# Performance work log

Measured on AMD Instinct MI355X. Metric: run time of the kernel, lower is better.

The kernel has to match this reference:

```python
import jax, jax.numpy as jnp
import numpy as np

B, T, EMB, H = 8, 1024, 128, 8


def setup_inputs() -> dict:
    key = jax.random.key(0)
    ks = jax.random.split(key, 7)
    s = 0.02
    return {
        "x": jax.random.normal(ks[0], (B, T, EMB), dtype=jnp.float32),
        "mask": jax.random.randint(ks[1], (1, T, T), 0, 2, dtype=jnp.int32),
        "Wk": (jax.random.normal(ks[2], (EMB * H, EMB), dtype=jnp.float32) * s),
        "Wq": (jax.random.normal(ks[3], (EMB * H, EMB), dtype=jnp.float32) * s),
        "Wv": (jax.random.normal(ks[4], (EMB * H, EMB), dtype=jnp.float32) * s),
        "Wu": (jax.random.normal(ks[5], (EMB, EMB * H), dtype=jnp.float32) * s),
        "bu": (jax.random.normal(ks[6], (EMB,), dtype=jnp.float32) * s),
    }


def reference(x, mask, Wk, Wq, Wv, Wu, bu):
    b, t, e = x.shape  # e == emb; per-head dim also == emb in this module
    h = Wk.shape[0] // e
    # projections: (b,t,e) @ (e, h*e) -> (b,t,h,e) -> (b,h,t,e)
    q = (x @ Wq.T).reshape(b, t, h, e).transpose(0, 2, 1, 3)
    k = (x @ Wk.T).reshape(b, t, h, e).transpose(0, 2, 1, 3)
    v = (x @ Wv.T).reshape(b, t, h, e).transpose(0, 2, 1, 3)
    scale = e ** 0.25  # torch scales q and k each by e**(1/4)
    dot = jnp.einsum('bhqe,bhke->bhqk', q / scale, k / scale)
    # causal mask: strictly-upper triangle (offset=1) set to -inf FIRST
    causal = jnp.triu(jnp.ones((t, t), dtype=bool), k=1)
    dot = jnp.where(causal, -jnp.inf, dot)
    # padding mask: where mask==0 set to -1e9 (overwrites -inf where overlapping)
    dot = jnp.where(mask[:, None] == 0, jnp.float32(-1e9), dot)
    attn = jax.nn.softmax(dot, axis=-1)
    out = jnp.einsum('bhqk,bhke->bhqe', attn, v)
    out = out.transpose(0, 2, 1, 3).reshape(b, t, h * e)
    return out @ Wu.T + bu
```

## Files before the change

### kernel.cpp

```cpp
#include <hip/hip_runtime.h>

#define Bn 8
#define Hn 8
#define Tn 1024
#define Dn 128

typedef __attribute__((ext_vector_type(8))) short bf16x8;
typedef __attribute__((ext_vector_type(4))) float f32x4;

typedef __attribute__((address_space(3))) unsigned int lds_as_t;
typedef __attribute__((address_space(1))) const unsigned int glb_as_t;

static __device__ __forceinline__ void gload_lds16(const unsigned short* g, unsigned short* l) {
    __builtin_amdgcn_global_load_lds((glb_as_t*)g, (lds_as_t*)l, 16, 0, 0);
}
static __device__ __forceinline__ void gload_lds16b(const char* g, char* l) {
    __builtin_amdgcn_global_load_lds((glb_as_t*)g, (lds_as_t*)l, 16, 0, 0);
}

static __device__ __forceinline__ unsigned short f2bf(float f) {
    union { float f; unsigned int u; } v; v.f = f;
    unsigned int u = v.u;
    return (unsigned short)((u + 0x7FFFu + ((u >> 16) & 1u)) >> 16);
}
static __device__ __forceinline__ int pack_bf16_trunc(float lo, float hi) {
    union { float f; unsigned int u; } a, b;
    a.f = lo; b.f = hi;
    return (int)__builtin_amdgcn_perm(b.u, a.u, 0x07060302u);
}

__global__ __launch_bounds__(256) void prep_kernel(
    const float* __restrict__ x,  const float* __restrict__ Wq,
    const float* __restrict__ Wk, const float* __restrict__ Wv,
    const float* __restrict__ Wu, const int* __restrict__ mask,
    const float* __restrict__ bu, float* __restrict__ outp,
    unsigned short* __restrict__ xb,  unsigned short* __restrict__ wqB,
    unsigned short* __restrict__ wkB, unsigned short* __restrict__ wvB,
    unsigned short* __restrict__ wuF, unsigned long long* __restrict__ bits)
{
    const int blk = blockIdx.x;
    const int tid = threadIdx.x;

    if (blk < 1408) {
        const float* in; unsigned short* out; int i4;
        if (blk < 1024)      { in = x;  out = xb;  i4 = blk * 256 + tid; }
        else if (blk < 1152) { in = Wq; out = wqB; i4 = (blk - 1024) * 256 + tid; }
        else if (blk < 1280) { in = Wk; out = wkB; i4 = (blk - 1152) * 256 + tid; }
        else                 { in = Wv; out = wvB; i4 = (blk - 1280) * 256 + tid; }
        float4 f = ((const float4*)in)[i4];
        ushort4 o;
        o.x = f2bf(f.x); o.y = f2bf(f.y); o.z = f2bf(f.z); o.w = f2bf(f.w);
        int base = i4 * 4;
        int row = base >> 7, col = base & 127;
        int scol = (((col >> 3) ^ (row & 15)) << 3) | (col & 7);
        *(ushort4*)(out + row * 128 + scol) = o;
    } else if (blk < 1536) {
        if (tid < 128) {
            int id = (blk - 1408) * 128 + tid;
            int lane_ = id & 63;
            int fid = id >> 6;
            int nt = fid & 7, ks = (fid >> 3) & 3, h = fid >> 5;
            int row = nt * 16 + (lane_ & 15);
            int col = h * 128 + ks * 32 + (lane_ >> 4) * 8;
            const float* src = Wu + (size_t)row * 1024 + col;
            float4 f0 = *(const float4*)(src);
            float4 f1 = *(const float4*)(src + 4);
            unsigned short o[8];
            o[0] = f2bf(f0.x); o[1] = f2bf(f0.y); o[2] = f2bf(f0.z); o[3] = f2bf(f0.w);
            o[4] = f2bf(f1.x); o[5] = f2bf(f1.y); o[6] = f2bf(f1.z); o[7] = f2bf(f1.w);
            *(ushort4*)(wuF + (size_t)id * 8)     = *(ushort4*)&o[0];
            *(ushort4*)(wuF + (size_t)id * 8 + 4) = *(ushort4*)&o[4];
        }
    } else if (blk < 2560) {
        int wid  = (blk - 1536) * 4 + (tid >> 6);
        int lane = tid & 63;
#pragma unroll
        for (int i = 0; i < 4; i++) {
            int widx = wid * 4 + i;
            int row = widx >> 4, kt = widx & 15;
            int v = mask[row * Tn + kt * 64 + lane];
            unsigned long long b = __ballot(v != 0);
            if (lane == 0) bits[kt * Tn + row] = b;
        }
    } else {
        int f4 = (blk - 2560) * 1024 + tid * 4;
#pragma unroll
        for (int i = 0; i < 4; i++)
            ((float4*)outp)[f4 + i] = ((const float4*)bu)[(f4 + i) & 31];
    }
}

__global__ __launch_bounds__(256, 1) void qkv_kernel(
    const unsigned short* __restrict__ xb,
    const unsigned short* __restrict__ wqB,
    const unsigned short* __restrict__ wkB,
    const unsigned short* __restrict__ wvB,
    char* __restrict__ Q,
    char* __restrict__ K,
    unsigned short* __restrict__ Vt)
{
    const int bx = blockIdx.x, by = blockIdx.y;
    const int wave = threadIdx.x >> 6;
    const int lane = threadIdx.x & 63;
    const int l16  = lane & 15;
    const int quad = lane >> 4;
    const int wm = wave & 1, wn = wave >> 1;

    __shared__ __align__(16) unsigned short As[128 * 128];
    __shared__ __align__(16) unsigned short Bs[3][128 * 128];
    __shared__ __align__(16) char escr[128 * 144];

    const unsigned short* Ag = xb + (size_t)bx * 128 * 128;
    const unsigned short* Bg0 = wqB + (size_t)by * 128 * 128;
    const unsigned short* Bg1 = wkB + (size_t)by * 128 * 128;
    const unsigned short* Bg2 = wvB + (size_t)by * 128 * 128;

#pragma unroll
    for (int i = 0; i < 8; i++) {
        int base = (wave * 8 + i) * 512;
        gload_lds16(Ag  + base + lane * 8, &As[base]);
        gload_lds16(Bg0 + base + lane * 8, &Bs[0][base]);
    }
    __syncthreads();

    bf16x8 a[4][4];
#pragma unroll
    for (int mt = 0; mt < 4; mt++) {
        int row = wm * 64 + mt * 16 + l16;
#pragma unroll
        for (int ks = 0; ks < 4; ks++)
            a[mt][ks] = *(const bf16x8*)(&As[row * 128 + (((ks * 4 + quad) ^ (row & 15)) << 3)]);
    }

    const int h_ = by;
    const int b_ = bx >> 3;
    f32x4 acc[4][4];

    {
#pragma unroll
        for (int i = 0; i < 8; i++) {
            int base = (wave * 8 + i) * 512;
            gload_lds16(Bg1 + base + lane * 8, &Bs[1][base]);
        }
#pragma unroll
        for (int nt = 0; nt < 4; nt++) {
            int row = wn * 64 + nt * 16 + l16;
            bf16x8 b4[4];
#pragma unroll
            for (int ks = 0; ks < 4; ks++)
                b4[ks] = *(const bf16x8*)(&Bs[0][row * 128 + (((ks * 4 + quad) ^ (row & 15)) << 3)]);
#pragma unroll
            for (int mt = 0; mt < 4; mt++) {
                f32x4 c = {0.f, 0.f, 0.f, 0.f};
#pragma unroll
                for (int ks = 0; ks < 4; ks++)
                    c = __builtin_amdgcn_mfma_f32_16x16x32_bf16(a[mt][ks], b4[ks], c, 0, 0, 0);
                acc[mt][nt] = c;
            }
        }
#pragma unroll
        for (int mt = 0; mt < 4; mt++) {
#pragma unroll
            for (int nt = 0; nt < 4; nt++) {
                int w = __builtin_amdgcn_cvt_pk_fp8_f32(acc[mt][nt][0], acc[mt][nt][1], 0, false);
                w = __builtin_amdgcn_cvt_pk_fp8_f32(acc[mt][nt][2], acc[mt][nt][3], w, true);
                int col = wn * 64 + nt * 16 + l16;
#pragma unroll
                for (int r = 0; r < 4; r++)
                    escr[(wm * 64 + mt * 16 + quad * 4 + r) * 144 + col] = (char)(w >> (8 * r));
            }
        }
        __syncthreads();
        const int f = threadIdx.x;
        int row = f >> 1;
        int t_in = (bx & 7) * 128 + row;
        size_t rowbase = ((size_t)((b_ * Hn + h_) * Tn + t_in)) * 128;
#pragma unroll
        for (int i = 0; i < 4; i++) {
            int c = (f & 1) * 4 + i;
            int4 v = *(const int4*)(escr + row * 144 + c * 16);
            *(int4*)(Q + rowbase + c * 16) = v;
        }
    }

    {
#pragma unroll
        for (int i = 0; i < 8; i++) {
            int base = (wave * 8 + i) * 512;
            gload_lds16(Bg2 + base + lane * 8, &Bs[2][base]);
        }
#pragma unroll
        for (int nt = 0; nt < 4; nt++) {
            int row = wn * 64 + nt * 16 + l16;
            bf16x8 b4[4];
#pragma unroll
            for (int ks = 0; ks < 4; ks++)
                b4[ks] = *(const bf16x8*)(&Bs[1][row * 128 + (((ks * 4 + quad) ^ (row & 15)) << 3)]);
#pragma unroll
            for (int mt = 0; mt < 4; mt++) {
                f32x4 c = {0.f, 0.f, 0.f, 0.f};
#pragma unroll
                for (int ks = 0; ks < 4; ks++)
                    c = __builtin_amdgcn_mfma_f32_16x16x32_bf16(a[mt][ks], b4[ks], c, 0, 0, 0);
                acc[mt][nt] = c;
            }
        }
        __syncthreads();
#pragma unroll
        for (int mt = 0; mt < 4; mt++) {
#pragma unroll
            for (int nt = 0; nt < 4; nt++) {
                int w = __builtin_amdgcn_cvt_pk_fp8_f32(acc[mt][nt][0], acc[mt][nt][1], 0, false);
                w = __builtin_amdgcn_cvt_pk_fp8_f32(acc[mt][nt][2], acc[mt][nt][3], w, true);
                int col = wn * 64 + nt * 16 + l16;
#pragma unroll
                for (int r = 0; r < 4; r++)
                    escr[(wm * 64 + mt * 16 + quad * 4 + r) * 144 + col] = (char)(w >> (8 * r));
            }
        }
        __syncthreads();
        const int f = threadIdx.x;
        int row = f >> 1;
        int t_in = (bx & 7) * 128 + row;
        size_t rowbase = ((size_t)((b_ * Hn + h_) * Tn + t_in)) * 128;
#pragma unroll
        for (int i = 0; i < 4; i++) {
            int c = (f & 1) * 4 + i;
            int4 v = *(const int4*)(escr + row * 144 + c * 16);
            int cc = c ^ (row & 7);
            *(int4*)(K + rowbase + cc * 16) = v;
        }
    }

    {
#pragma unroll
        for (int nt = 0; nt < 4; nt++) {
            int row = wn * 64 + nt * 16 + l16;
            bf16x8 b4[4];
#pragma unroll
            for (int ks = 0; ks < 4; ks++)
                b4[ks] = *(const bf16x8*)(&Bs[2][row * 128 + (((ks * 4 + quad) ^ (row & 15)) << 3)]);
#pragma unroll
            for (int mt = 0; mt < 4; mt++) {
                f32x4 c = {0.f, 0.f, 0.f, 0.f};
#pragma unroll
                for (int ks = 0; ks < 4; ks++)
                    c = __builtin_amdgcn_mfma_f32_16x16x32_bf16(a[mt][ks], b4[ks], c, 0, 0, 0);
                acc[mt][nt] = c;
            }
        }
#pragma unroll
        for (int mt = 0; mt < 4; mt++) {
            int m_base = bx * 128 + wm * 64 + mt * 16 + quad * 4;
            int t0 = m_base & 1023;
#pragma unroll
            for (int nt = 0; nt < 4; nt++) {
                int e_ = wn * 64 + nt * 16 + l16;
                int kt_ = t0 >> 6, tc0 = t0 & 63;
                size_t off = ((((size_t)(b_ * Hn + h_) * 16 + kt_) * 128 + e_) << 6)
                           + ((((tc0 >> 3) ^ (e_ & 7)) << 3) | (tc0 & 7));
                ushort4 v4;
                v4.x = f2bf(acc[mt][nt][0]); v4.y = f2bf(acc[mt][nt][1]);
                v4.z = f2bf(acc[mt][nt][2]); v4.w = f2bf(acc[mt][nt][3]);
                *(ushort4*)(Vt + off) = v4;
            }
        }
    }
}

__global__ __launch_bounds__(256, 2) void attn_kernel(
    const char* __restrict__ Q,
    const char* __restrict__ K,
    const unsigned short* __restrict__ Vt,
    const unsigned long long* __restrict__ mbits,
    const unsigned short* __restrict__ wuF,
    float* __restrict__ out)
{
    const int id   = blockIdx.x;
    const int qb   = (id & 7) ^ (7 * ((id >> 8) & 1));
    const int bh   = (id >> 3) & 63;
    const int wave = threadIdx.x >> 6;
    const int lane = threadIdx.x & 63;
    const int l16  = lane & 15;
    const int quad = lane >> 4;

    __shared__ __align__(16) char kbuf[2][64 * 128];
    __shared__ __align__(16) unsigned short vbuf[2][128 * 64];

    const char* Qb = Q  + (size_t)bh * Tn * Dn;
    const char* Kb = K  + (size_t)bh * Tn * Dn;
    const unsigned short* Vb = Vt + (size_t)bh * (16 * 128 * 64);

    const int blkkt = 2 * qb + 1;
    const int q0w   = qb * 128 + wave * 32;
    const int q0s[2] = { q0w, q0w + 16 };
    const int wkmax = (q0w + 31) >> 6;

    long qf[2][4];
#pragma unroll
    for (int st = 0; st < 2; st++)
#pragma unroll
        for (int ks = 0; ks < 4; ks++)
            qf[st][ks] = *(const long*)(Qb + (size_t)(q0s[st] + l16) * 128 + ks * 32 + quad * 8);

    bf16x8 ones;
#pragma unroll
    for (int j = 0; j < 8; j++) ones[j] = (short)0x3F80;

    f32x4 o[2][8];
#pragma unroll
    for (int st = 0; st < 2; st++)
#pragma unroll
        for (int et = 0; et < 8; et++) o[st][et] = (f32x4){0.f, 0.f, 0.f, 0.f};
    f32x4 lacc[2];
    lacc[0] = (f32x4){0.f, 0.f, 0.f, 0.f};
    lacc[1] = (f32x4){0.f, 0.f, 0.f, 0.f};

    const float SL = 0.12752041570284543f;

    const int idx0 = (l16 << 2) + ((quad & 1) << 7);
    const int idx1 = idx0 + 64;
    const bool hiQ = (quad >> 1) != 0;

#pragma unroll
    for (int i = 0; i < 2; i++) {
        int base = (wave * 2 + i) * 1024;
        gload_lds16b(Kb + base + lane * 16, &kbuf[0][base]);
    }
#pragma unroll
    for (int i = 0; i < 4; i++) {
        int base = (wave * 4 + i) * 512;
        gload_lds16(Vb + base + lane * 8, &vbuf[0][base]);
    }

    for (int kt = 0; kt <= blkkt; kt++) {
        const int cur = kt & 1;
        __syncthreads();

        if (kt < blkkt) {
            const char* Kg = Kb + (kt + 1) * (64 * 128);
            const unsigned short* Vg = Vb + (kt + 1) * (128 * 64);
#pragma unroll
            for (int i = 0; i < 2; i++) {
                int base = (wave * 2 + i) * 1024;
                gload_lds16b(Kg + base + lane * 16, &kbuf[cur ^ 1][base]);
            }
#pragma unroll
            for (int i = 0; i < 4; i++) {
                int base = (wave * 4 + i) * 512;
                gload_lds16(Vg + base + lane * 8, &vbuf[cur ^ 1][base]);
            }
        }

        if (kt <= wkmax) {
            unsigned long long mw[2];
            mw[0] = mbits[kt * Tn + q0s[0] + l16];
            mw[1] = mbits[kt * Tn + q0s[1] + l16];

            f32x4 s[2][4];
#pragma unroll
            for (int nt = 0; nt < 4; nt++) {
                int row = nt * 16 + l16;
                long a4[4];
#pragma unroll
                for (int ks = 0; ks < 4; ks++) {
                    int c = ks * 2 + (quad >> 1);
                    a4[ks] = *(const long*)(&kbuf[cur][row * 128 + (((c ^ (row & 7)) << 4) | ((quad & 1) << 3))]);
                }
#pragma unroll
                for (int st = 0; st < 2; st++) {
                    f32x4 c = {0.f, 0.f, 0.f, 0.f};
#pragma unroll
                    for (int ks = 0; ks < 4; ks++)
                        c = __builtin_amdgcn_mfma_f32_16x16x32_fp8_fp8(a4[ks], qf[st][ks], c, 0, 0, 0);
                    s[st][nt] = c;
                }
            }

            const int kc0 = kt * 64;
            bf16x8 pf[2][2];
#pragma unroll
            for (int st = 0; st < 2; st++) {
                const int qglob = q0s[st] + l16;
                int w[4][2];
#pragma unroll
                for (int nt = 0; nt < 4; nt++) {
                    float pv[4];
#pragma unroll
                    for (int r = 0; r < 4; r++) {
                        int bit = nt * 16 + quad * 4 + r;
                        bool live = ((mw[st] >> bit) & 1ULL) && (kc0 + bit <= qglob);
                        pv[r] = live ? __builtin_amdgcn_exp2f(s[st][nt][r] * SL) : 0.f;
                    }
                    w[nt][0] = pack_bf16_trunc(pv[0], pv[1]);
                    w[nt][1] = pack_bf16_trunc(pv[2], pv[3]);
                }
#pragma unroll
                for (int k2 = 0; k2 < 2; k2++) {
                    union { int i[4]; bf16x8 v; } u;
#pragma unroll
                    for (int d = 0; d < 4; d++) {
                        int idx = (d < 2) ? idx0 : idx1;
                        int va = __builtin_amdgcn_ds_bpermute(idx, w[2 * k2][d & 1]);
                        int vb = __builtin_amdgcn_ds_bpermute(idx, w[2 * k2 + 1][d & 1]);
                        u.i[d] = hiQ ? vb : va;
                    }
                    pf[st][k2] = u.v;
                }
            }

#pragma unroll
            for (int st = 0; st < 2; st++)
#pragma unroll
                for (int k2 = 0; k2 < 2; k2++)
                    lacc[st] = __builtin_amdgcn_mfma_f32_16x16x32_bf16(pf[st][k2], ones, lacc[st], 0, 0, 0);

#pragma unroll
            for (int et = 0; et < 8; et++) {
                int row = et * 16 + l16;
#pragma unroll
                for (int k2 = 0; k2 < 2; k2++) {
                    bf16x8 b = *(const bf16x8*)(&vbuf[cur][row * 64 + (((k2 * 4 + quad) ^ (l16 & 7)) << 3)]);
                    o[0][et] = __builtin_amdgcn_mfma_f32_16x16x32_bf16(pf[0][k2], b, o[0][et], 0, 0, 0);
                    o[1][et] = __builtin_amdgcn_mfma_f32_16x16x32_bf16(pf[1][k2], b, o[1][et], 0, 0, 0);
                }
            }
        }
    }

    __syncthreads();
    {
        bool deg = false;
#pragma unroll
        for (int st = 0; st < 2; st++)
#pragma unroll
            for (int r = 0; r < 4; r++) deg |= (lacc[st][r] == 0.f);
        if (__ballot(deg) != 0ULL) {
            unsigned short* pb = (unsigned short*)((char*)kbuf + wave * 2304);
            unsigned short dsel[2][4];
#pragma unroll
            for (int st = 0; st < 2; st++)
#pragma unroll
                for (int r = 0; r < 4; r++)
                    dsel[st][r] = (lacc[st][r] == 0.f) ? (unsigned short)0x3F80 : (unsigned short)0;
            for (int kt = 0; kt < 16; kt++) {
#pragma unroll
                for (int st = 0; st < 2; st++) {
                    int qrow = q0s[st] + quad * 4;
                    unsigned long long mw2[4];
#pragma unroll
                    for (int r = 0; r < 4; r++) mw2[r] = mbits[kt * Tn + qrow + r];
#pragma unroll
                    for (int nt = 0; nt < 4; nt++) {
                        int bi = nt * 16 + l16;
#pragma unroll
                        for (int r = 0; r < 4; r++)
                            pb[(quad * 4 + r) * 72 + bi] = ((mw2[r] >> bi) & 1ULL) ? (unsigned short)0 : dsel[st][r];
                    }
                    bf16x8 pf[2];
#pragma unroll
                    for (int k2 = 0; k2 < 2; k2++)
                        pf[k2] = *(const bf16x8*)(&pb[l16 * 72 + k2 * 32 + quad * 8]);
#pragma unroll
                    for (int k2 = 0; k2 < 2; k2++)
                        lacc[st] = __builtin_amdgcn_mfma_f32_16x16x32_bf16(pf[k2], ones, lacc[st], 0, 0, 0);
                    const unsigned short* Vg = Vb + kt * (128 * 64);
#pragma unroll
                    for (int et = 0; et < 8; et++) {
#pragma unroll
                        for (int k2 = 0; k2 < 2; k2++) {
                            bf16x8 b = *(const bf16x8*)(Vg + (et * 16 + l16) * 64 + (((k2 * 4 + quad) ^ (l16 & 7)) << 3));
                            o[st][et] = __builtin_amdgcn_mfma_f32_16x16x32_bf16(pf[k2], b, o[st][et], 0, 0, 0);
                        }
                    }
                }
            }
        }
    }

    const int b_ = bh >> 3, h_ = bh & 7;
    const unsigned short* wf = wuF + (size_t)h_ * (4 * 8 * 64 * 8);
#pragma unroll
    for (int st = 0; st < 2; st++) {
        unsigned short* tile = (unsigned short*)((char*)vbuf + wave * 4608);
#pragma unroll
        for (int r = 0; r < 4; r++) {
            float inv = 1.f / lacc[st][r];
            int row = quad * 4 + r;
#pragma unroll
            for (int et = 0; et < 8; et++)
                tile[row * 144 + et * 16 + l16] = f2bf(o[st][et][r] * inv);
        }

        bf16x8 a4[4];
#pragma unroll
        for (int ks = 0; ks < 4; ks++)
            a4[ks] = *(const bf16x8*)(&tile[l16 * 144 + ks * 32 + quad * 8]);

        f32x4 acc2[8];
#pragma unroll
        for (int nt = 0; nt < 8; nt++) acc2[nt] = (f32x4){0.f, 0.f, 0.f, 0.f};
#pragma unroll
        for (int ks = 0; ks < 4; ks++) {
#pragma unroll
            for (int nt = 0; nt < 8; nt++) {
                bf16x8 b = *(const bf16x8*)(wf + ((size_t)(ks * 8 + nt) * 64 + lane) * 8);
                acc2[nt] = __builtin_amdgcn_mfma_f32_16x16x32_bf16(a4[ks], b, acc2[nt], 0, 0, 0);
            }
        }

#pragma unroll
        for (int nt = 0; nt < 8; nt++) {
            int n = nt * 16 + l16;
#pragma unroll
            for (int r = 0; r < 4; r++) {
                int q = q0s[st] + quad * 4 + r;
                atomicAdd(&out[(size_t)(b_ * Tn + q) * Dn + n], acc2[nt][r]);
            }
        }
    }
}

extern "C" void kernel_launch(void* const* d_in, const int* in_sizes, int n_in,
                              void* d_out, int out_size, void* d_ws, size_t ws_size,
                              hipStream_t stream) {
    const float* x   = (const float*)d_in[0];
    const int* mask  = (const int*)d_in[1];
    const float* Wk  = (const float*)d_in[2];
    const float* Wq  = (const float*)d_in[3];
    const float* Wv  = (const float*)d_in[4];
    const float* Wu  = (const float*)d_in[5];
    const float* bu  = (const float*)d_in[6];
    float* out = (float*)d_out;

    char* ws = (char*)d_ws;
    unsigned short* xb  = (unsigned short*)ws; ws += (size_t)8192 * 128 * 2;
    unsigned short* wqB = (unsigned short*)ws; ws += (size_t)1024 * 128 * 2;
    unsigned short* wkB = (unsigned short*)ws; ws += (size_t)1024 * 128 * 2;
    unsigned short* wvB = (unsigned short*)ws; ws += (size_t)1024 * 128 * 2;
    unsigned short* wuF = (unsigned short*)ws; ws += (size_t)128 * 1024 * 2;
    char* Qf  = ws; ws += (size_t)64 * 1024 * 128;
    char* Kf  = ws; ws += (size_t)64 * 1024 * 128;
    unsigned short* Vtw = (unsigned short*)ws; ws += (size_t)64 * 1024 * 128 * 2;
    unsigned long long* mb = (unsigned long long*)ws; ws += (size_t)1024 * 16 * 8;

    prep_kernel<<<dim3(2816), 256, 0, stream>>>(x, Wq, Wk, Wv, Wu, mask, bu, out,
                                                xb, wqB, wkB, wvB, wuF, mb);
    qkv_kernel<<<dim3(64, 8), 256, 0, stream>>>(xb, wqB, wkB, wvB, Qf, Kf, Vtw);
    attn_kernel<<<dim3(512), 256, 0, stream>>>(Qf, Kf, Vtw, mb, wuF, out);
}
```

Measured before the change: 147.7 us.

## Fuse prep, QKV projection and attention into one persistent kernel with grid barriers

Merges the three launches into a single persistent kernel of 512 blocks that loops over the prep work, then the QKV projection work items, then attention, separated by flag-based grid barriers. The QKV stage is split into 1536 work items (one weight matrix each) instead of 512 items that each computed Q, K and V, which lowers LDS use so two blocks can be resident per CU. The aim is to remove launch gaps and tail effects between kernels. It relies on all 512 blocks being co-resident; the barrier tokens are fixed constants and the flags are never reset, so the barriers can pass immediately on a second call if the workspace keeps the old values. Launch bounds of 2 blocks per CU may also cap registers for the attention stage.

Result: slower. 497.4 us (+236.8%).

```diff
diff --git a/kernel.cpp b/kernel.cpp
--- a/kernel.cpp
+++ b/kernel.cpp
@@ -29,493 +29,431 @@
     return (int)__builtin_amdgcn_perm(b.u, a.u, 0x07060302u);
 }
 
-__global__ __launch_bounds__(256) void prep_kernel(
+static __device__ __forceinline__ void grid_barrier(unsigned* flags, unsigned token) {
+    __syncthreads();
+    __threadfence();
+    if (threadIdx.x == 0)
+        __hip_atomic_store(&flags[blockIdx.x], token, __ATOMIC_RELEASE, __HIP_MEMORY_SCOPE_AGENT);
+    const int i0 = threadIdx.x, i1 = threadIdx.x + 256;
+    while (__hip_atomic_load(&flags[i0], __ATOMIC_ACQUIRE, __HIP_MEMORY_SCOPE_AGENT) != token)
+        __builtin_amdgcn_s_sleep(1);
+    while (__hip_atomic_load(&flags[i1], __ATOMIC_ACQUIRE, __HIP_MEMORY_SCOPE_AGENT) != token)
+        __builtin_amdgcn_s_sleep(1);
+    __syncthreads();
+    __threadfence();
+}
+
+__global__ __launch_bounds__(256, 2) void mega_kernel(
     const float* __restrict__ x,  const float* __restrict__ Wq,
     const float* __restrict__ Wk, const float* __restrict__ Wv,
     const float* __restrict__ Wu, const int* __restrict__ mask,
-    const float* __restrict__ bu, float* __restrict__ outp,
+    const float* __restrict__ bu, float* __restrict__ out,
     unsigned short* __restrict__ xb,  unsigned short* __restrict__ wqB,
     unsigned short* __restrict__ wkB, unsigned short* __restrict__ wvB,
-    unsigned short* __restrict__ wuF, unsigned long long* __restrict__ bits)
+    unsigned short* __restrict__ wuF, char* __restrict__ Qf,
+    char* __restrict__ Kf, unsigned short* __restrict__ Vtw,
+    unsigned long long* __restrict__ mbits, unsigned* __restrict__ flags)
 {
-    const int blk = blockIdx.x;
-    const int tid = threadIdx.x;
-
-    if (blk < 1408) {
-        const float* in; unsigned short* out; int i4;
-        if (blk < 1024)      { in = x;  out = xb;  i4 = blk * 256 + tid; }
-        else if (blk < 1152) { in = Wq; out = wqB; i4 = (blk - 1024) * 256 + tid; }
-        else if (blk < 1280) { in = Wk; out = wkB; i4 = (blk - 1152) * 256 + tid; }
-        else                 { in = Wv; out = wvB; i4 = (blk - 1280) * 256 + tid; }
-        float4 f = ((const float4*)in)[i4];
-        ushort4 o;
-        o.x = f2bf(f.x); o.y = f2bf(f.y); o.z = f2bf(f.z); o.w = f2bf(f.w);
-        int base = i4 * 4;
-        int row = base >> 7, col = base & 127;
-        int scol = (((col >> 3) ^ (row & 15)) << 3) | (col & 7);
-        *(ushort4*)(out + row * 128 + scol) = o;
-    } else if (blk < 1536) {
-        if (tid < 128) {
-            int id = (blk - 1408) * 128 + tid;
-            int lane_ = id & 63;
-            int fid = id >> 6;
-            int nt = fid & 7, ks = (fid >> 3) & 3, h = fid >> 5;
-            int row = nt * 16 + (lane_ & 15);
-            int col = h * 128 + ks * 32 + (lane_ >> 4) * 8;
-            const float* src = Wu + (size_t)row * 1024 + col;
-            float4 f0 = *(const float4*)(src);
-            float4 f1 = *(const float4*)(src + 4);
-            unsigned short o[8];
-            o[0] = f2bf(f0.x); o[1] = f2bf(f0.y); o[2] = f2bf(f0.z); o[3] = f2bf(f0.w);
-            o[4] = f2bf(f1.x); o[5] = f2bf(f1.y); o[6] = f2bf(f1.z); o[7] = f2bf(f1.w);
-            *(ushort4*)(wuF + (size_t)id * 8)     = *(ushort4*)&o[0];
-            *(ushort4*)(wuF + (size_t)id * 8 + 4) = *(ushort4*)&o[4];
-        }
-    } else if (blk < 2560) {
-        int wid  = (blk - 1536) * 4 + (tid >> 6);
-        int lane = tid & 63;
-#pragma unroll
-        for (int i = 0; i < 4; i++) {
-            int widx = wid * 4 + i;
-            int row = widx >> 4, kt = widx & 15;
-            int v = mask[row * Tn + kt * 64 + lane];
-            unsigned long long b = __ballot(v != 0);
-            if (lane == 0) bits[kt * Tn + row] = b;
-        }
-    } else {
-        int f4 = (blk - 2560) * 1024 + tid * 4;
-#pragma unroll
-        for (int i = 0; i < 4; i++)
-            ((float4*)outp)[f4 + i] = ((const float4*)bu)[(f4 + i) & 31];
-    }
-}
-
-__global__ __launch_bounds__(256, 1) void qkv_kernel(
-    const unsigned short* __restrict__ xb,
-    const unsigned short* __restrict__ wqB,
-    const unsigned short* __restrict__ wkB,
-    const unsigned short* __restrict__ wvB,
-    char* __restrict__ Q,
-    char* __restrict__ K,
-    unsigned short* __restrict__ Vt)
-{
-    const int bx = blockIdx.x, by = blockIdx.y;
-    const int wave = threadIdx.x >> 6;
-    const int lane = threadIdx.x & 63;
+    __shared__ __align__(16) char shm[65536];
+
+    const int gid  = blockIdx.x;
+    const int tid  = threadIdx.x;
+    const int wave = tid >> 6;
+    const int lane = tid & 63;
     const int l16  = lane & 15;
     const int quad = lane >> 4;
-    const int wm = wave & 1, wn = wave >> 1;
-
-    __shared__ __align__(16) unsigned short As[128 * 128];
-    __shared__ __align__(16) unsigned short Bs[3][128 * 128];
-    __shared__ __align__(16) char escr[128 * 144];
-
-    const unsigned short* Ag = xb + (size_t)bx * 128 * 128;
-    const unsigned short* Bg0 = wqB + (size_t)by * 128 * 128;
-    const unsigned short* Bg1 = wkB + (size_t)by * 128 * 128;
-    const unsigned short* Bg2 = wvB + (size_t)by * 128 * 128;
-
-#pragma unroll
-    for (int i = 0; i < 8; i++) {
-        int base = (wave * 8 + i) * 512;
-        gload_lds16(Ag  + base + lane * 8, &As[base]);
-        gload_lds16(Bg0 + base + lane * 8, &Bs[0][base]);
+
+    for (int blk = gid; blk < 2816; blk += 512) {
+        if (blk < 1408) {
+            const float* in; unsigned short* o_; int i4;
+            if (blk < 1024)      { in = x;  o_ = xb;  i4 = blk * 256 + tid; }
+            else if (blk < 1152) { in = Wq; o_ = wqB; i4 = (blk - 1024) * 256 + tid; }
+            else if (blk < 1280) { in = Wk; o_ = wkB; i4 = (blk - 1152) * 256 + tid; }
+            else                 { in = Wv; o_ = wvB; i4 = (blk - 1280) * 256 + tid; }
+            float4 f = ((const float4*)in)[i4];
+            ushort4 o;
+            o.x = f2bf(f.x); o.y = f2bf(f.y); o.z = f2bf(f.z); o.w = f2bf(f.w);
+            int base = i4 * 4;
+            int row = base >> 7, col = base & 127;
+            int scol = (((col >> 3) ^ (row & 15)) << 3) | (col & 7);
+            *(ushort4*)(o_ + row * 128 + scol) = o;
+        } else if (blk < 1536) {
+            if (tid < 128) {
+                int id = (blk - 1408) * 128 + tid;
+                int lane_ = id & 63;
+                int fid = id >> 6;
+                int nt = fid & 7, ks = (fid >> 3) & 3, h = fid >> 5;
+                int row = nt * 16 + (lane_ & 15);
+                int col = h * 128 + ks * 32 + (lane_ >> 4) * 8;
+                const float* src = Wu + (size_t)row * 1024 + col;
+                float4 f0 = *(const float4*)(src);
+                float4 f1 = *(const float4*)(src + 4);
+                unsigned short o[8];
+                o[0] = f2bf(f0.x); o[1] = f2bf(f0.y); o[2] = f2bf(f0.z); o[3] = f2bf(f0.w);
+                o[4] = f2bf(f1.x); o[5] = f2bf(f1.y); o[6] = f2bf(f1.z); o[7] = f2bf(f1.w);
+                *(ushort4*)(wuF + (size_t)id * 8)     = *(ushort4*)&o[0];
+                *(ushort4*)(wuF + (size_t)id * 8 + 4) = *(ushort4*)&o[4];
+            }
+        } else if (blk < 2560) {
+            int wid  = (blk - 1536) * 4 + (tid >> 6);
+#pragma unroll
+            for (int i = 0; i < 4; i++) {
+                int widx = wid * 4 + i;
+                int row = widx >> 4, kt = widx & 15;
+                int v = mask[row * Tn + kt * 64 + lane];
+                unsigned long long b = __ballot(v != 0);
+                if (lane == 0) mbits[kt * Tn + row] = b;
+            }
+        } else {
+            int f4 = (blk - 2560) * 1024 + tid * 4;
+#pragma unroll
+            for (int i = 0; i < 4; i++)
+                ((float4*)out)[f4 + i] = ((const float4*)bu)[(f4 + i) & 31];
+        }
     }
-    __syncthreads();
-
-    bf16x8 a[4][4];
-#pragma unroll
-    for (int mt = 0; mt < 4; mt++) {
-        int row = wm * 64 + mt * 16 + l16;
-#pragma unroll
-        for (int ks = 0; ks < 4; ks++)
-            a[mt][ks] = *(const bf16x8*)(&As[row * 128 + (((ks * 4 + quad) ^ (row & 15)) << 3)]);
+
+    grid_barrier(flags, 0x11111111u);
+
+    {
+        unsigned short* As = (unsigned short*)shm;
+        unsigned short* Bs = (unsigned short*)(shm + 32768);
+        const int wm = wave & 1, wn = wave >> 1;
+
+        for (int it = 0; it < 3; it++) {
+            const int wi = gid + it * 512;
+            const int bx = wi & 63, by = wi >> 6;
+            __syncthreads();
+
+            const int which = by >> 3;
+            const unsigned short* wsel = (which == 0) ? wqB : (which == 1) ? wkB : wvB;
+            const unsigned short* Ag = xb + (size_t)bx * 128 * 128;
+            const unsigned short* Bg = wsel + (size_t)(by & 7) * 128 * 128;
+
+#pragma unroll
+            for (int i = 0; i < 8; i++) {
+                int base = (wave * 8 + i) * 512;
+                gload_lds16(Ag + base + lane * 8, &As[base]);
+                gload_lds16(Bg + base + lane * 8, &Bs[base]);
+            }
+            __syncthreads();
+
+            bf16x8 a[4][4];
+#pragma unroll
+            for (int mt = 0; mt < 4; mt++) {
+                int row = wm * 64 + mt * 16 + l16;
+#pragma unroll
+                for (int ks = 0; ks < 4; ks++)
+                    a[mt][ks] = *(const bf16x8*)(&As[row * 128 + (((ks * 4 + quad) ^ (row & 15)) << 3)]);
+            }
+
+            f32x4 acc[4][4];
+#pragma unroll
+            for (int nt = 0; nt < 4; nt++) {
+                int row = wn * 64 + nt * 16 + l16;
+                bf16x8 b4[4];
+#pragma unroll
+                for (int ks = 0; ks < 4; ks++)
+                    b4[ks] = *(const bf16x8*)(&Bs[row * 128 + (((ks * 4 + quad) ^ (row & 15)) << 3)]);
+#pragma unroll
+                for (int mt = 0; mt < 4; mt++) {
+                    f32x4 c = {0.f, 0.f, 0.f, 0.f};
+#pragma unroll
+                    for (int ks = 0; ks < 4; ks++)
+                        c = __builtin_amdgcn_mfma_f32_16x16x32_bf16(a[mt][ks], b4[ks], c, 0, 0, 0);
+                    acc[mt][nt] = c;
+                }
+            }
+
+            const int h_ = by & 7;
+            const int b_ = bx >> 3;
+            if (which < 2) {
+                __syncthreads();
+                char* escr = shm;
+#pragma unroll
+                for (int mt = 0; mt < 4; mt++) {
+#pragma unroll
+                    for (int nt = 0; nt < 4; nt++) {
+                        int w = __builtin_amdgcn_cvt_pk_fp8_f32(acc[mt][nt][0], acc[mt][nt][1], 0, false);
+                        w = __builtin_amdgcn_cvt_pk_fp8_f32(acc[mt][nt][2], acc[mt][nt][3], w, true);
+                        int col = wn * 64 + nt * 16 + l16;
+#pragma unroll
+                        for (int r = 0; r < 4; r++)
+                            escr[(wm * 64 + mt * 16 + quad * 4 + r) * 144 + col] = (char)(w >> (8 * r));
+                    }
+                }
+                __syncthreads();
+                int row = tid >> 1;
+                int t_in = (bx & 7) * 128 + row;
+                char* dst = (which == 0) ? Qf : Kf;
+                size_t rowbase = ((size_t)((b_ * Hn + h_) * Tn + t_in)) * 128;
+#pragma unroll
+                for (int i = 0; i < 4; i++) {
+                    int c = (tid & 1) * 4 + i;
+                    int4 v = *(const int4*)(escr + row * 144 + c * 16);
+                    int cc = (which == 1) ? (c ^ (row & 7)) : c;
+                    *(int4*)(dst + rowbase + cc * 16) = v;
+                }
+            } else {
+#pragma unroll
+                for (int mt = 0; mt < 4; mt++) {
+                    int m_base = bx * 128 + wm * 64 + mt * 16 + quad * 4;
+                    int t0 = m_base & 1023;
+#pragma unroll
+                    for (int nt = 0; nt < 4; nt++) {
+                        int e_ = wn * 64 + nt * 16 + l16;
+                        int kt_ = t0 >> 6, tc0 = t0 & 63;
+                        size_t off = ((((size_t)(b_ * Hn + h_) * 16 + kt_) * 128 + e_) << 6)
+                                   + ((((tc0 >> 3) ^ (e_ & 7)) << 3) | (tc0 & 7));
+                        ushort4 v4;
+                        v4.x = f2bf(acc[mt][nt][0]); v4.y = f2bf(acc[mt][nt][1]);
+                        v4.z = f2bf(acc[mt][nt][2]); v4.w = f2bf(acc[mt][nt][3]);
+                        *(ushort4*)(Vtw + off) = v4;
+                    }
+                }
+            }
+        }
     }
 
-    const int h_ = by;
-    const int b_ = bx >> 3;
-    f32x4 acc[4][4];
+    grid_barrier(flags, 0x22222222u);
 
     {
-#pragma unroll
-        for (int i = 0; i < 8; i++) {
-            int base = (wave * 8 + i) * 512;
-            gload_lds16(Bg1 + base + lane * 8, &Bs[1][base]);
-        }
-#pragma unroll
-        for (int nt = 0; nt < 4; nt++) {
-            int row = wn * 64 + nt * 16 + l16;
-            bf16x8 b4[4];
+        char* kb = shm;
+        unsigned short* vb = (unsigned short*)(shm + 16384);
+
+        const int id   = gid;
+        const int qb   = (id & 7) ^ (7 * ((id >> 8) & 1));
+        const int bh   = (id >> 3) & 63;
+
+        const char* Qb = Qf + (size_t)bh * Tn * Dn;
+        const char* Kb = Kf + (size_t)bh * Tn * Dn;
+        const unsigned short* Vb = Vtw + (size_t)bh * (16 * 128 * 64);
+
+        const int blkkt = 2 * qb + 1;
+        const int q0w   = qb * 128 + wave * 32;
+        const int q0s[2] = { q0w, q0w + 16 };
+        const int wkmax = (q0w + 31) >> 6;
+
+        long qf[2][4];
+#pragma unroll
+        for (int st = 0; st < 2; st++)
 #pragma unroll
             for (int ks = 0; ks < 4; ks++)
-                b4[ks] = *(const bf16x8*)(&Bs[0][row * 128 + (((ks * 4 + quad) ^ (row & 15)) << 3)]);
-#pragma unroll
-            for (int mt = 0; mt < 4; mt++) {
-                f32x4 c = {0.f, 0.f, 0.f, 0.f};
-#pragma unroll
-                for (int ks = 0; ks < 4; ks++)
-                    c = __builtin_amdgcn_mfma_f32_16x16x32_bf16(a[mt][ks], b4[ks], c, 0, 0, 0);
-                acc[mt][nt] = c;
-            }
-        }
-#pragma unroll
-        for (int mt = 0; mt < 4; mt++) {
-#pragma unroll
-            for (int nt = 0; nt < 4; nt++) {
-                int w = __builtin_amdgcn_cvt_pk_fp8_f32(acc[mt][nt][0], acc[mt][nt][1], 0, false);
-                w = __builtin_amdgcn_cvt_pk_fp8_f32(acc[mt][nt][2], acc[mt][nt][3], w, true);
-                int col = wn * 64 + nt * 16 + l16;
-#pragma unroll
-                for (int r = 0; r < 4; r++)
-                    escr[(wm * 64 + mt * 16 + quad * 4 + r) * 144 + col] = (char)(w >> (8 * r));
-            }
-        }
+                qf[st][ks] = *(const long*)(Qb + (size_t)(q0s[st] + l16) * 128 + ks * 32 + quad * 8);
+
+        bf16x8 ones;
+#pragma unroll
+        for (int j = 0; j < 8; j++) ones[j] = (short)0x3F80;
+
+        f32x4 o[2][8];
+#pragma unroll
+        for (int st = 0; st < 2; st++)
+#pragma unroll
+            for (int et = 0; et < 8; et++) o[st][et] = (f32x4){0.f, 0.f, 0.f, 0.f};
+        f32x4 lacc[2];
+        lacc[0] = (f32x4){0.f, 0.f, 0.f, 0.f};
+        lacc[1] = (f32x4){0.f, 0.f, 0.f, 0.f};
+
+        const float SL = 0.12752041570284543f;
+
+        const int idx0 = (l16 << 2) + ((quad & 1) << 7);
+        const int idx1 = idx0 + 64;
+        const bool hiQ = (quad >> 1) != 0;
+
+#pragma unroll
+        for (int i = 0; i < 2; i++) {
+            int base = (wave * 2 + i) * 1024;
+            gload_lds16b(Kb + base + lane * 16, &kb[base]);
+        }
+#pragma unroll
+        for (int i = 0; i < 4; i++) {
+            int base = (wave * 4 + i) * 512;
+            gload_lds16(Vb + base + lane * 8, &vb[base]);
+        }
+
+        for (int kt = 0; kt <= blkkt; kt++) {
+            const int cur = kt & 1;
+            __syncthreads();
+
+            if (kt < blkkt) {
+                const char* Kg = Kb + (kt + 1) * (64 * 128);
+                const unsigned short* Vg = Vb + (kt + 1) * (128 * 64);
+#pragma unroll
+                for (int i = 0; i < 2; i++) {
+                    int base = (wave * 2 + i) * 1024;
+                    gload_lds16b(Kg + base + lane * 16, &kb[(cur ^ 1) * 8192 + base]);
+                }
+#pragma unroll
+                for (int i = 0; i < 4; i++) {
+                    int base = (wave * 4 + i) * 512;
+                    gload_lds16(Vg + base + lane * 8, &vb[(cur ^ 1) * 8192 + base]);
+                }
+            }
+
+            if (kt <= wkmax) {
+                unsigned long long mw[2];
+                mw[0] = mbits[kt * Tn + q0s[0] + l16];
+                mw[1] = mbits[kt * Tn + q0s[1] + l16];
+
+                f32x4 s[2][4];
+#pragma unroll
+                for (int nt = 0; nt < 4; nt++) {
+                    int row = nt * 16 + l16;
+                    long a4[4];
+#pragma unroll
+                    for (int ks = 0; ks < 4; ks++) {
+                        int c = ks * 2 + (quad >> 1);
+                        a4[ks] = *(const long*)(&kb[cur * 8192 + row * 128 + (((c ^ (row & 7)) << 4) | ((quad & 1) << 3))]);
+                    }
+#pragma unroll
+                    for (int st = 0; st < 2; st++) {
+                        f32x4 c = {0.f, 0.f, 0.f, 0.f};
+#pragma unroll
+                        for (int ks = 0; ks < 4; ks++)
+                            c = __builtin_amdgcn_mfma_f32_16x16x32_fp8_fp8(a4[ks], qf[st][ks], c, 0, 0, 0);
+                        s[st][nt] = c;
+                    }
+                }
+
+                const int kc0 = kt * 64;
+                bf16x8 pf[2][2];
+#pragma unroll
+                for (int st = 0; st < 2; st++) {
+                    const int qglob = q0s[st] + l16;
+                    int w[4][2];
+#pragma unroll
+                    for (int nt = 0; nt < 4; nt++) {
+                        float pv[4];
+#pragma unroll
+                        for (int r = 0; r < 4; r++) {
+                            int bit = nt * 16 + quad * 4 + r;
+                            bool live = ((mw[st] >> bit) & 1ULL) && (kc0 + bit <= qglob);
+                            pv[r] = live ? __builtin_amdgcn_exp2f(s[st][nt][r] * SL) : 0.f;
+                        }
+                        w[nt][0] = pack_bf16_trunc(pv[0], pv[1]);
+                        w[nt][1] = pack_bf16_trunc(pv[2], pv[3]);
+                    }
+#pragma unroll
+                    for (int k2 = 0; k2 < 2; k2++) {
+                        union { int i[4]; bf16x8 v; } u;
+#pragma unroll
+                        for (int d = 0; d < 4; d++) {
+                            int idx = (d < 2) ? idx0 : idx1;
+                            int va = __builtin_amdgcn_ds_bpermute(idx, w[2 * k2][d & 1]);
+                            int vvb = __builtin_amdgcn_ds_bpermute(idx, w[2 * k2 + 1][d & 1]);
+                            u.i[d] = hiQ ? vvb : va;
+                        }
+                        pf[st][k2] = u.v;
+                    }
+                }
+
+#pragma unroll
+                for (int st = 0; st < 2; st++)
+#pragma unroll
+                    for (int k2 = 0; k2 < 2; k2++)
+                        lacc[st] = __builtin_amdgcn_mfma_f32_16x16x32_bf16(pf[st][k2], ones, lacc[st], 0, 0, 0);
+
+#pragma unroll
+                for (int et = 0; et < 8; et++) {
+                    int row = et * 16 + l16;
+#pragma unroll
+                    for (int k2 = 0; k2 < 2; k2++) {
+                        bf16x8 b = *(const bf16x8*)(&vb[cur * 8192 + row * 64 + (((k2 * 4 + quad) ^ (l16 & 7)) << 3)]);
+                        o[0][et] = __builtin_amdgcn_mfma_f32_16x16x32_bf16(pf[0][k2], b, o[0][et], 0, 0, 0);
+                        o[1][et] = __builtin_amdgcn_mfma_f32_16x16x32_bf16(pf[1][k2], b, o[1][et], 0, 0, 0);
+                    }
+                }
+            }
+        }
+
         __syncthreads();
-        const int f = threadIdx.x;
-        int row = f >> 1;
-        int t_in = (bx & 7) * 128 + row;
-        size_t rowbase = ((size_t)((b_ * Hn + h_) * Tn + t_in)) * 128;
-#pragma unroll
-        for (int i = 0; i < 4; i++) {
-            int c = (f & 1) * 4 + i;
-            int4 v = *(const int4*)(escr + row * 144 + c * 16);
-            *(int4*)(Q + rowbase + c * 16) = v;
-        }
-    }
-
-    {
-#pragma unroll
-        for (int i = 0; i < 8; i++) {
-            int base = (wave * 8 + i) * 512;
-            gload_lds16(Bg2 + base + lane * 8, &Bs[2][base]);
-        }
-#pragma unroll
-        for (int nt = 0; nt < 4; nt++) {
-            int row = wn * 64 + nt * 16 + l16;
-            bf16x8 b4[4];
+        {
+            bool deg = false;
+#pragma unroll
+            for (int st = 0; st < 2; st++)
+#pragma unroll
+                for (int r = 0; r < 4; r++) deg |= (lacc[st][r] == 0.f);
+            if (__ballot(deg) != 0ULL) {
+                unsigned short* pb = (unsigned short*)(shm + wave * 2304);
+                unsigned short dsel[2][4];
+#pragma unroll
+                for (int st = 0; st < 2; st++)
+#pragma unroll
+                    for (int r = 0; r < 4; r++)
+                        dsel[st][r] = (lacc[st][r] == 0.f) ? (unsigned short)0x3F80 : (unsigned short)0;
+                for (int kt = 0; kt < 16; kt++) {
+#pragma unroll
+                    for (int st = 0; st < 2; st++) {
+                        int qrow = q0s[st] + quad * 4;
+                        unsigned long long mw2[4];
+#pragma unroll
+                        for (int r = 0; r < 4; r++) mw2[r] = mbits[kt * Tn + qrow + r];
+#pragma unroll
+                        for (int nt = 0; nt < 4; nt++) {
+                            int bi = nt * 16 + l16;
+#pragma unroll
+                            for (int r = 0; r < 4; r++)
+                                pb[(quad * 4 + r) * 72 + bi] = ((mw2[r] >> bi) & 1ULL) ? (unsigned short)0 : dsel[st][r];
+                        }
+                        bf16x8 pf[2];
+#pragma unroll
+                        for (int k2 = 0; k2 < 2; k2++)
+                            pf[k2] = *(const bf16x8*)(&pb[l16 * 72 + k2 * 32 + quad * 8]);
+#pragma unroll
+                        for (int k2 = 0; k2 < 2; k2++)
+                            lacc[st] = __builtin_amdgcn_mfma_f32_16x16x32_bf16(pf[k2], ones, lacc[st], 0, 0, 0);
+                        const unsigned short* Vg = Vb + kt * (128 * 64);
+#pragma unroll
+                        for (int et = 0; et < 8; et++) {
+#pragma unroll
+                            for (int k2 = 0; k2 < 2; k2++) {
+                                bf16x8 b = *(const bf16x8*)(Vg + (et * 16 + l16) * 64 + (((k2 * 4 + quad) ^ (l16 & 7)) << 3));
+                                o[st][et] = __builtin_amdgcn_mfma_f32_16x16x32_bf16(pf[k2], b, o[st][et], 0, 0, 0);
+                            }
+                        }
+                    }
+                }
+            }
+        }
+
+        const int b_ = bh >> 3, h_ = bh & 7;
+        const unsigned short* wf = wuF + (size_t)h_ * (4 * 8 * 64 * 8);
+#pragma unroll
+        for (int st = 0; st < 2; st++) {
+            unsigned short* tile = (unsigned short*)(shm + 16384 + wave * 4608);
+#pragma unroll
+            for (int r = 0; r < 4; r++) {
+                float inv = 1.f / lacc[st][r];
+                int row = quad * 4 + r;
+#pragma unroll
+                for (int et = 0; et < 8; et++)
+                    tile[row * 144 + et * 16 + l16] = f2bf(o[st][et][r] * inv);
+            }
+
+            bf16x8 a4[4];
 #pragma unroll
             for (int ks = 0; ks < 4; ks++)
-                b4[ks] = *(const bf16x8*)(&Bs[1][row * 128 + (((ks * 4 + quad) ^ (row & 15)) << 3)]);
-#pragma unroll
-            for (int mt = 0; mt < 4; mt++) {
-                f32x4 c = {0.f, 0.f, 0.f, 0.f};
-#pragma unroll
-                for (int ks = 0; ks < 4; ks++)
-                    c = __builtin_amdgcn_mfma_f32_16x16x32_bf16(a[mt][ks], b4[ks], c, 0, 0, 0);
-                acc[mt][nt] = c;
-            }
-        }
-        __syncthreads();
-#pragma unroll
-        for (int mt = 0; mt < 4; mt++) {
-#pragma unroll
-            for (int nt = 0; nt < 4; nt++) {
-                int w = __builtin_amdgcn_cvt_pk_fp8_f32(acc[mt][nt][0], acc[mt][nt][1], 0, false);
-                w = __builtin_amdgcn_cvt_pk_fp8_f32(acc[mt][nt][2], acc[mt][nt][3], w, true);
-                int col = wn * 64 + nt * 16 + l16;
-#pragma unroll
-                for (int r = 0; r < 4; r++)
-                    escr[(wm * 64 + mt * 16 + quad * 4 + r) * 144 + col] = (char)(w >> (8 * r));
-            }
-        }
-        __syncthreads();
-        const int f = threadIdx.x;
-        int row = f >> 1;
-        int t_in = (bx & 7) * 128 + row;
-        size_t rowbase = ((size_t)((b_ * Hn + h_) * Tn + t_in)) * 128;
-#pragma unroll
-        for (int i = 0; i < 4; i++) {
-            int c = (f & 1) * 4 + i;
-            int4 v = *(const int4*)(escr + row * 144 + c * 16);
-            int cc = c ^ (row & 7);
-            *(int4*)(K + rowbase + cc * 16) = v;
-        }
-    }
-
-    {
-#pragma unroll
-        for (int nt = 0; nt < 4; nt++) {
-            int row = wn * 64 + nt * 16 + l16;
-            bf16x8 b4[4];
-#pragma unroll
-            for (int ks = 0; ks < 4; ks++)
-                b4[ks] = *(const bf16x8*)(&Bs[2][row * 128 + (((ks * 4 + quad) ^ (row & 15)) << 3)]);
-#pragma unroll
-            for (int mt = 0; mt < 4; mt++) {
-                f32x4 c = {0.f, 0.f, 0.f, 0.f};
-#pragma unroll
-                for (int ks = 0; ks < 4; ks++)
-                    c = __builtin_amdgcn_mfma_f32_16x16x32_bf16(a[mt][ks], b4[ks], c, 0, 0, 0);
-                acc[mt][nt] = c;
-            }
-        }
-#pragma unroll
-        for (int mt = 0; mt < 4; mt++) {
-            int m_base = bx * 128 + wm * 64 + mt * 16 + quad * 4;
-            int t0 = m_base & 1023;
-#pragma unroll
-            for (int nt = 0; nt < 4; nt++) {
-                int e_ = wn * 64 + nt * 16 + l16;
-                int kt_ = t0 >> 6, tc0 = t0 & 63;
-                size_t off = ((((size_t)(b_ * Hn + h_) * 16 + kt_) * 128 + e_) << 6)
-                           + ((((tc0 >> 3) ^ (e_ & 7)) << 3) | (tc0 & 7));
-                ushort4 v4;
-                v4.x = f2bf(acc[mt][nt][0]); v4.y = f2bf(acc[mt][nt][1]);
-                v4.z = f2bf(acc[mt][nt][2]); v4.w = f2bf(acc[mt][nt][3]);
-                *(ushort4*)(Vt + off) = v4;
-            }
-        }
-    }
-}
-
-__global__ __launch_bounds__(256, 2) void attn_kernel(
-    const char* __restrict__ Q,
-    const char* __restrict__ K,
-    const unsigned short* __restrict__ Vt,
-    const unsigned long long* __restrict__ mbits,
-    const unsigned short* __restrict__ wuF,
-    float* __restrict__ out)
-{
-    const int id   = blockIdx.x;
-    const int qb   = (id & 7) ^ (7 * ((id >> 8) & 1));
-    const int bh   = (id >> 3) & 63;
-    const int wave = threadIdx.x >> 6;
-    const int lane = threadIdx.x & 63;
-    const int l16  = lane & 15;
-    const int quad = lane >> 4;
-
-    __shared__ __align__(16) char kbuf[2][64 * 128];
-    __shared__ __align__(16) unsigned short vbuf[2][128 * 64];
-
-    const char* Qb = Q  + (size_t)bh * Tn * Dn;
-    const char* Kb = K  + (size_t)bh * Tn * Dn;
-    const unsigned short* Vb = Vt + (size_t)bh * (16 * 128 * 64);
-
-    const int blkkt = 2 * qb + 1;
-    const int q0w   = qb * 128 + wave * 32;
-    const int q0s[2] = { q0w, q0w + 16 };
-    const int wkmax = (q0w + 31) >> 6;
-
-    long qf[2][4];
-#pragma unroll
-    for (int st = 0; st < 2; st++)
-#pragma unroll
-        for (int ks = 0; ks < 4; ks++)
-            qf[st][ks] = *(const long*)(Qb + (size_t)(q0s[st] + l16) * 128 + ks * 32 + quad * 8);
-
-    bf16x8 ones;
-#pragma unroll
-    for (int j = 0; j < 8; j++) ones[j] = (short)0x3F80;
-
-    f32x4 o[2][8];
-#pragma unroll
-    for (int st = 0; st < 2; st++)
-#pragma unroll
-        for (int et = 0; et < 8; et++) o[st][et] = (f32x4){0.f, 0.f, 0.f, 0.f};
-    f32x4 lacc[2];
-    lacc[0] = (f32x4){0.f, 0.f, 0.f, 0.f};
-    lacc[1] = (f32x4){0.f, 0.f, 0.f, 0.f};
-
-    const float SL = 0.12752041570284543f;
-
-    const int idx0 = (l16 << 2) + ((quad & 1) << 7);
-    const int idx1 = idx0 + 64;
-    const bool hiQ = (quad >> 1) != 0;
-
-#pragma unroll
-    for (int i = 0; i < 2; i++) {
-        int base = (wave * 2 + i) * 1024;
-        gload_lds16b(Kb + base + lane * 16, &kbuf[0][base]);
-    }
-#pragma unroll
-    for (int i = 0; i < 4; i++) {
-        int base = (wave * 4 + i) * 512;
-        gload_lds16(Vb + base + lane * 8, &vbuf[0][base]);
-    }
-
-    for (int kt = 0; kt <= blkkt; kt++) {
-        const int cur = kt & 1;
-        __syncthreads();
-
-        if (kt < blkkt) {
-            const char* Kg = Kb + (kt + 1) * (64 * 128);
-            const unsigned short* Vg = Vb + (kt + 1) * (128 * 64);
-#pragma unroll
-            for (int i = 0; i < 2; i++) {
-                int base = (wave * 2 + i) * 1024;
-                gload_lds16b(Kg + base + lane * 16, &kbuf[cur ^ 1][base]);
-            }
-#pragma unroll
-            for (int i = 0; i < 4; i++) {
-                int base = (wave * 4 + i) * 512;
-                gload_lds16(Vg + base + lane * 8, &vbuf[cur ^ 1][base]);
-            }
-        }
-
-        if (kt <= wkmax) {
-            unsigned long long mw[2];
-            mw[0] = mbits[kt * Tn + q0s[0] + l16];
-            mw[1] = mbits[kt * Tn + q0s[1] + l16];
-
-            f32x4 s[2][4];
-#pragma unroll
-            for (int nt = 0; nt < 4; nt++) {
-                int row = nt * 16 + l16;
-                long a4[4];
-#pragma unroll
-                for (int ks = 0; ks < 4; ks++) {
-                    int c = ks * 2 + (quad >> 1);
-                    a4[ks] = *(const long*)(&kbuf[cur][row * 128 + (((c ^ (row & 7)) << 4) | ((quad & 1) << 3))]);
-                }
-#pragma unroll
-                for (int st = 0; st < 2; st++) {
-                    f32x4 c = {0.f, 0.f, 0.f, 0.f};
-#pragma unroll
-                    for (int ks = 0; ks < 4; ks++)
-                        c = __builtin_amdgcn_mfma_f32_16x16x32_fp8_fp8(a4[ks], qf[st][ks], c, 0, 0, 0);
-                    s[st][nt] = c;
-                }
-            }
-
-            const int kc0 = kt * 64;
-            bf16x8 pf[2][2];
-#pragma unroll
-            for (int st = 0; st < 2; st++) {
-                const int qglob = q0s[st] + l16;
-                int w[4][2];
-#pragma unroll
-                for (int nt = 0; nt < 4; nt++) {
-                    float pv[4];
-#pragma unroll
-                    for (int r = 0; r < 4; r++) {
-                        int bit = nt * 16 + quad * 4 + r;
-                        bool live = ((mw[st] >> bit) & 1ULL) && (kc0 + bit <= qglob);
-                        pv[r] = live ? __builtin_amdgcn_exp2f(s[st][nt][r] * SL) : 0.f;
-                    }
-                    w[nt][0] = pack_bf16_trunc(pv[0], pv[1]);
-                    w[nt][1] = pack_bf16_trunc(pv[2], pv[3]);
-                }
-#pragma unroll
-                for (int k2 = 0; k2 < 2; k2++) {
-                    union { int i[4]; bf16x8 v; } u;
-#pragma unroll
-                    for (int d = 0; d < 4; d++) {
-                        int idx = (d < 2) ? idx0 : idx1;
-                        int va = __builtin_amdgcn_ds_bpermute(idx, w[2 * k2][d & 1]);
-                        int vb = __builtin_amdgcn_ds_bpermute(idx, w[2 * k2 + 1][d & 1]);
-                        u.i[d] = hiQ ? vb : va;
-                    }
-                    pf[st][k2] = u.v;
-                }
-            }
-
-#pragma unroll
-            for (int st = 0; st < 2; st++)
-#pragma unroll
-                for (int k2 = 0; k2 < 2; k2++)
-                    lacc[st] = __builtin_amdgcn_mfma_f32_16x16x32_bf16(pf[st][k2], ones, lacc[st], 0, 0, 0);
-
-#pragma unroll
-            for (int et = 0; et < 8; et++) {
-                int row = et * 16 + l16;
-#pragma unroll
-                for (int k2 = 0; k2 < 2; k2++) {
-                    bf16x8 b = *(const bf16x8*)(&vbuf[cur][row * 64 + (((k2 * 4 + quad) ^ (l16 & 7)) << 3)]);
-                    o[0][et] = __builtin_amdgcn_mfma_f32_16x16x32_bf16(pf[0][k2], b, o[0][et], 0, 0, 0);
-                    o[1][et] = __builtin_amdgcn_mfma_f32_16x16x32_bf16(pf[1][k2], b, o[1][et], 0, 0, 0);
-                }
-            }
-        }
-    }
-
-    __syncthreads();
-    {
-        bool deg = false;
-#pragma unroll
-        for (int st = 0; st < 2; st++)
-#pragma unroll
-            for (int r = 0; r < 4; r++) deg |= (lacc[st][r] == 0.f);
-        if (__ballot(deg) != 0ULL) {
-            unsigned short* pb = (unsigned short*)((char*)kbuf + wave * 2304);
-            unsigned short dsel[2][4];
-#pragma unroll
-            for (int st = 0; st < 2; st++)
-#pragma unroll
-                for (int r = 0; r < 4; r++)
-                    dsel[st][r] = (lacc[st][r] == 0.f) ? (unsigned short)0x3F80 : (unsigned short)0;
-            for (int kt = 0; kt < 16; kt++) {
-#pragma unroll
-                for (int st = 0; st < 2; st++) {
-                    int qrow = q0s[st] + quad * 4;
-                    unsigned long long mw2[4];
-#pragma unroll
-                    for (int r = 0; r < 4; r++) mw2[r] = mbits[kt * Tn + qrow + r];
-#pragma unroll
-                    for (int nt = 0; nt < 4; nt++) {
-                        int bi = nt * 16 + l16;
-#pragma unroll
-                        for (int r = 0; r < 4; r++)
-                            pb[(quad * 4 + r) * 72 + bi] = ((mw2[r] >> bi) & 1ULL) ? (unsigned short)0 : dsel[st][r];
-                    }
-                    bf16x8 pf[2];
-#pragma unroll
-                    for (int k2 = 0; k2 < 2; k2++)
-                        pf[k2] = *(const bf16x8*)(&pb[l16 * 72 + k2 * 32 + quad * 8]);
-#pragma unroll
-                    for (int k2 = 0; k2 < 2; k2++)
-                        lacc[st] = __builtin_amdgcn_mfma_f32_16x16x32_bf16(pf[k2], ones, lacc[st], 0, 0, 0);
-                    const unsigned short* Vg = Vb + kt * (128 * 64);
-#pragma unroll
-                    for (int et = 0; et < 8; et++) {
-#pragma unroll
-                        for (int k2 = 0; k2 < 2; k2++) {
-                            bf16x8 b = *(const bf16x8*)(Vg + (et * 16 + l16) * 64 + (((k2 * 4 + quad) ^ (l16 & 7)) << 3));
-                            o[st][et] = __builtin_amdgcn_mfma_f32_16x16x32_bf16(pf[k2], b, o[st][et], 0, 0, 0);
-                        }
-                    }
-                }
-            }
-        }
-    }
-
-    const int b_ = bh >> 3, h_ = bh & 7;
-    const unsigned short* wf = wuF + (size_t)h_ * (4 * 8 * 64 * 8);
-#pragma unroll
-    for (int st = 0; st < 2; st++) {
-        unsigned short* tile = (unsigned short*)((char*)vbuf + wave * 4608);
-#pragma unroll
-        for (int r = 0; r < 4; r++) {
-            float inv = 1.f / lacc[st][r];
-            int row = quad * 4 + r;
-#pragma unroll
-            for (int et = 0; et < 8; et++)
-                tile[row * 144 + et * 16 + l16] = f2bf(o[st][et][r] * inv);
-        }
-
-        bf16x8 a4[4];
-#pragma unroll
-        for (int ks = 0; ks < 4; ks++)
-            a4[ks] = *(const bf16x8*)(&tile[l16 * 144 + ks * 32 + quad * 8]);
-
-        f32x4 acc2[8];
-#pragma unroll
-        for (int nt = 0; nt < 8; nt++) acc2[nt] = (f32x4){0.f, 0.f, 0.f, 0.f};
-#pragma unroll
-        for (int ks = 0; ks < 4; ks++) {
+                a4[ks] = *(const bf16x8*)(&tile[l16 * 144 + ks * 32 + quad * 8]);
+
+            f32x4 acc2[8];
+#pragma unroll
+            for (int nt = 0; nt < 8; nt++) acc2[nt] = (f32x4){0.f, 0.f, 0.f, 0.f};
+#pragma unroll
+            for (int ks = 0; ks < 4; ks++) {
+#pragma unroll
+                for (int nt = 0; nt < 8; nt++) {
+                    bf16x8 b = *(const bf16x8*)(wf + ((size_t)(ks * 8 + nt) * 64 + lane) * 8);
+                    acc2[nt] = __builtin_amdgcn_mfma_f32_16x16x32_bf16(a4[ks], b, acc2[nt], 0, 0, 0);
+                }
+            }
+
 #pragma unroll
             for (int nt = 0; nt < 8; nt++) {
-                bf16x8 b = *(const bf16x8*)(wf + ((size_t)(ks * 8 + nt) * 64 + lane) * 8);
-                acc2[nt] = __builtin_amdgcn_mfma_f32_16x16x32_bf16(a4[ks], b, acc2[nt], 0, 0, 0);
-            }
-        }
-
-#pragma unroll
-        for (int nt = 0; nt < 8; nt++) {
-            int n = nt * 16 + l16;
-#pragma unroll
-            for (int r = 0; r < 4; r++) {
-                int q = q0s[st] + quad * 4 + r;
-                atomicAdd(&out[(size_t)(b_ * Tn + q) * Dn + n], acc2[nt][r]);
+                int n = nt * 16 + l16;
+#pragma unroll
+                for (int r = 0; r < 4; r++) {
+                    int q = q0s[st] + quad * 4 + r;
+                    atomicAdd(&out[(size_t)(b_ * Tn + q) * Dn + n], acc2[nt][r]);
+                }
             }
         }
     }
@@ -543,9 +481,9 @@
     char* Kf  = ws; ws += (size_t)64 * 1024 * 128;
     unsigned short* Vtw = (unsigned short*)ws; ws += (size_t)64 * 1024 * 128 * 2;
     unsigned long long* mb = (unsigned long long*)ws; ws += (size_t)1024 * 16 * 8;
-
-    prep_kernel<<<dim3(2816), 256, 0, stream>>>(x, Wq, Wk, Wv, Wu, mask, bu, out,
-                                                xb, wqB, wkB, wvB, wuF, mb);
-    qkv_kernel<<<dim3(64, 8), 256, 0, stream>>>(xb, wqB, wkB, wvB, Qf, Kf, Vtw);
-    attn_kernel<<<dim3(512), 256, 0, stream>>>(Qf, Kf, Vtw, mb, wuF, out);
-}
+    unsigned* flags = (unsigned*)ws; ws += 512 * 4;
+
+    mega_kernel<<<dim3(512), dim3(256), 0, stream>>>(
+        x, Wq, Wk, Wv, Wu, mask, bu, out,
+        xb, wqB, wkB, wvB, wuF, Qf, Kf, Vtw, mb, flags);
+}
```
